# Optimization experiments

Measured on AMD Instinct MI355X. Metric: run time of the kernel, lower is better.

## Reference

```python
import jax, jax.numpy as jnp
import numpy as np

N = 50000      # nodes of type 'student'
E = 625000     # edges per relation
H = 128        # hidden_channels
C = 6          # num_classes
F_IN = 3       # hardcoded num_features in the module


def setup_inputs() -> dict:
    key = jax.random.key(0)
    ks = jax.random.split(key, 32)
    s = 0.05
    d = {}
    d["x_student"] = jax.random.normal(ks[0], (N, F_IN), dtype=jnp.float32)
    d["ei_friend"] = jax.random.randint(ks[1], (2, E), 0, N)
    d["ei_study"] = jax.random.randint(ks[2], (2, E), 0, N)
    # embedding Linear(3 -> H)
    d["emb_w"] = jax.random.normal(ks[3], (F_IN, H), dtype=jnp.float32) * s
    d["emb_b"] = jnp.zeros((H,), jnp.float32)
    # per-layer, per-edge-type RGCNConv params: relation-0 weight, root weight, bias
    i = 4
    for l in range(2):
        for e in ("f", "s"):
            d[f"w_rel_{l}_{e}"] = jax.random.normal(ks[i], (H, H), dtype=jnp.float32) * s; i += 1
            d[f"w_root_{l}_{e}"] = jax.random.normal(ks[i], (H, H), dtype=jnp.float32) * s; i += 1
            d[f"b_{l}_{e}"] = jnp.zeros((H,), jnp.float32)
    # output Linear(H -> C)
    d["out_w"] = jax.random.normal(ks[i], (H, C), dtype=jnp.float32) * s
    d["out_b"] = jnp.zeros((C,), jnp.float32)
    return d


def _rgcn_conv(h, ei, w_rel, w_root, b):
    # PyG RGCNConv with edge_type==0 everywhere: mean-aggregate src features at dst,
    # project by relation-0 weight, add root transform and bias.
    src, dst = ei[0], ei[1]
    msg = h[src]                                             # [E, H] gather
    agg = jax.ops.segment_sum(msg, dst, num_segments=N)      # [N, H]
    deg = jax.ops.segment_sum(jnp.ones((ei.shape[1],), h.dtype), dst, num_segments=N)
    agg = agg / jnp.maximum(deg, 1.0)[:, None]               # mean aggr (0 for isolated nodes)
    return agg @ w_rel + h @ w_root + b


def reference(x_student, ei_friend, ei_study, emb_w, emb_b,
              w_rel_0_f, w_root_0_f, b_0_f, w_rel_0_s, w_root_0_s, b_0_s,
              w_rel_1_f, w_root_1_f, b_1_f, w_rel_1_s, w_root_1_s, b_1_s,
              out_w, out_b):
    h = jax.nn.relu(x_student @ emb_w + emb_b)
    # layer 0: sum over the two relations, divide by valid_edge_count=2, relu (dropout eval=no-op)
    acc = _rgcn_conv(h, ei_friend, w_rel_0_f, w_root_0_f, b_0_f) \
        + _rgcn_conv(h, ei_study, w_rel_0_s, w_root_0_s, b_0_s)
    h = jax.nn.relu(acc / 2.0)
    # layer 1 (last): no relu/dropout
    acc = _rgcn_conv(h, ei_friend, w_rel_1_f, w_root_1_f, b_1_f) \
        + _rgcn_conv(h, ei_study, w_rel_1_s, w_root_1_s, b_1_s)
    h = acc / 2.0
    return h @ out_w + out_b
```

## Files before the change

kernel.cpp:

```cpp
#include <hip/hip_runtime.h>

#define NN 50000
#define NE 625000
#define HD 128
#define CAP 40
#define ZROW NN

typedef __attribute__((ext_vector_type(8))) short short8;
typedef __attribute__((ext_vector_type(4))) float f32x4;
typedef __attribute__((ext_vector_type(4))) unsigned uint4v;

__device__ __forceinline__ unsigned short f2bf(float f) {
    unsigned u = __builtin_bit_cast(unsigned, f);
    u += 0x7FFFu + ((u >> 16) & 1u);
    return (unsigned short)(u >> 16);
}
__device__ __forceinline__ unsigned pack2(float lo, float hi) {
    return (unsigned)f2bf(lo) | ((unsigned)f2bf(hi) << 16);
}
__device__ __forceinline__ float bflo(unsigned v) { unsigned u = v << 16; return __builtin_bit_cast(float, u); }
__device__ __forceinline__ float bfhi(unsigned v) { unsigned u = v & 0xFFFF0000u; return __builtin_bit_cast(float, u); }

__device__ __forceinline__ void extract8(uint4v u, int j0, int cnt, unsigned* out) {
    unsigned raw[8];
    raw[0] = u.x & 0xFFFFu; raw[1] = u.x >> 16;
    raw[2] = u.y & 0xFFFFu; raw[3] = u.y >> 16;
    raw[4] = u.z & 0xFFFFu; raw[5] = u.z >> 16;
    raw[6] = u.w & 0xFFFFu; raw[7] = u.w >> 16;
    #pragma unroll
    for (int j = 0; j < 8; ++j) out[j] = (j0 + j < cnt) ? raw[j] : ZROW;
}

__global__ __launch_bounds__(256) void k_prep(
    const float* __restrict__ x, const float* __restrict__ w,
    const float* __restrict__ b, unsigned* __restrict__ h0, unsigned* __restrict__ h1,
    const int* __restrict__ ei_f, const int* __restrict__ ei_s,
    int* __restrict__ degF, int* __restrict__ degS,
    unsigned short* __restrict__ bktF, unsigned short* __restrict__ bktS,
    const float* __restrict__ wrf0, const float* __restrict__ wtf0, const float* __restrict__ bf0,
    const float* __restrict__ wrs0, const float* __restrict__ wts0, const float* __restrict__ bs0,
    const float* __restrict__ wrf1, const float* __restrict__ wtf1, const float* __restrict__ bf1,
    const float* __restrict__ wrs1, const float* __restrict__ wts1, const float* __restrict__ bs1,
    unsigned short* __restrict__ Wt, float* __restrict__ bcat)
{
    int bid = blockIdx.x, t = threadIdx.x;
    if (bid < 3920) {
        int rel = bid >= 1960;
        int bqq = bid - rel * 1960;
        int cls = bqq & 7;
        int chunk = bqq >> 3;
        const int* ei; int* deg; unsigned short* bkt;
        if (rel == 0) { ei = ei_f; deg = degF; bkt = bktF; }
        else          { ei = ei_s; deg = degS; bkt = bktS; }
        const int lo = cls * 6250, hi = lo + 6250;
        int e0 = chunk * 2560 + t;
        #pragma unroll
        for (int i = 0; i < 10; ++i) {
            int e = e0 + i * 256;
            if (e >= NE) continue;
            int d = ei[NE + e];
            if (d >= lo && d < hi) {
                int s = ei[e];
                int pos = atomicAdd(&deg[d], 1);
                if (pos < CAP) bkt[d*CAP + pos] = (unsigned short)s;
            }
        }
    } else if (bid < 16420) {
        int i = (bid - 3920) * 256 + t;
        int n = i >> 6, c = (i & 63) * 2;
        float x0 = x[n*3+0], x1 = x[n*3+1], x2 = x[n*3+2];
        float v0 = fmaf(x0, w[c],   fmaf(x1, w[HD+c],   fmaf(x2, w[2*HD+c],   b[c])));
        float v1 = fmaf(x0, w[c+1], fmaf(x1, w[HD+c+1], fmaf(x2, w[2*HD+c+1], b[c+1])));
        v0 = fmaxf(v0, 0.f); v1 = fmaxf(v1, 0.f);
        h0[i] = pack2(v0, v1);
    } else if (bid == 16420) {
        if (t < 64)       h0[(long)ZROW*64 + t] = 0u;
        else if (t < 128) h1[(long)ZROW*64 + (t - 64)] = 0u;
    } else {
        int i = (bid - 16421) * 256 + t;
        int ln = i / 384, k = i - ln * 384;
        int l = ln >> 7, n = ln & 127;
        const float* wrf = l ? wrf1 : wrf0;
        const float* wrs = l ? wrs1 : wrs0;
        const float* wtf = l ? wtf1 : wtf0;
        const float* wts = l ? wts1 : wts0;
        float v;
        if (k < 128)      v = wrf[k*HD + n];
        else if (k < 256) v = wrs[(k-128)*HD + n];
        else              v = wtf[(k-256)*HD + n] + wts[(k-256)*HD + n];
        Wt[(long)ln*384 + k] = f2bf(0.5f * v);
        if (i < 256) {
            int ll = i >> 7, cc = i & 127;
            const float* bfp = ll ? bf1 : bf0;
            const float* bsp = ll ? bs1 : bs0;
            bcat[i] = 0.5f * (bfp[cc] + bsp[cc]);
        }
    }
}

__global__ __launch_bounds__(256) void k_spmm(
    const unsigned* __restrict__ h,
    const int* __restrict__ degF, const int* __restrict__ degS,
    const unsigned short* __restrict__ bktF, const unsigned short* __restrict__ bktS,
    unsigned* __restrict__ aggF, unsigned* __restrict__ aggS)
{
    int w = threadIdx.x >> 6, lane = threadIdx.x & 63;
    int n = blockIdx.x * 4 + w;
    int dF = degF[n], dS = degS[n];
    int cF = min(dF, CAP), cS = min(dS, CAP);
    const unsigned short* rowF = bktF + (long)n*CAP;
    const unsigned short* rowS = bktS + (long)n*CAP;
    uint4v uF0 = *(const uint4v*)(rowF);
    uint4v uF1 = *(const uint4v*)(rowF + 8);
    uint4v uS0 = *(const uint4v*)(rowS);
    uint4v uS1 = *(const uint4v*)(rowS + 8);
    unsigned iF[16], iS[16];
    extract8(uF0, 0, cF, iF); extract8(uF1, 8, cF, iF + 8);
    extract8(uS0, 0, cS, iS); extract8(uS1, 8, cS, iS + 8);
    unsigned vF[16], vS[16];
    #pragma unroll
    for (int j = 0; j < 16; ++j) vF[j] = h[iF[j]*64u + lane];
    #pragma unroll
    for (int j = 0; j < 16; ++j) vS[j] = h[iS[j]*64u + lane];
    float aF0 = 0.f, aF1 = 0.f, aS0 = 0.f, aS1 = 0.f;
    #pragma unroll
    for (int j = 0; j < 16; ++j) { aF0 += bflo(vF[j]); aF1 += bfhi(vF[j]); }
    #pragma unroll
    for (int j = 0; j < 16; ++j) { aS0 += bflo(vS[j]); aS1 += bfhi(vS[j]); }
    for (int j = 16; j < cF; j += 8) {
        uint4v u = *(const uint4v*)(rowF + j);
        unsigned ii[8];
        extract8(u, j, cF, ii);
        unsigned vv[8];
        #pragma unroll
        for (int q = 0; q < 8; ++q) vv[q] = h[ii[q]*64u + lane];
        #pragma unroll
        for (int q = 0; q < 8; ++q) { aF0 += bflo(vv[q]); aF1 += bfhi(vv[q]); }
    }
    for (int j = 16; j < cS; j += 8) {
        uint4v u = *(const uint4v*)(rowS + j);
        unsigned ii[8];
        extract8(u, j, cS, ii);
        unsigned vv[8];
        #pragma unroll
        for (int q = 0; q < 8; ++q) vv[q] = h[ii[q]*64u + lane];
        #pragma unroll
        for (int q = 0; q < 8; ++q) { aS0 += bflo(vv[q]); aS1 += bfhi(vv[q]); }
    }
    float invF = 1.f / fmaxf((float)dF, 1.f);
    float invS = 1.f / fmaxf((float)dS, 1.f);
    aggF[n*64 + lane] = pack2(aF0*invF, aF1*invF);
    aggS[n*64 + lane] = pack2(aS0*invS, aS1*invS);
}

__global__ __launch_bounds__(256) void k_gemm(
    const unsigned short* __restrict__ A0, const unsigned short* __restrict__ A1,
    const unsigned short* __restrict__ A2,
    const unsigned short* __restrict__ Wt, const float* __restrict__ bias,
    unsigned short* __restrict__ outH, int mode,
    const float* __restrict__ ow, const float* __restrict__ ob,
    float* __restrict__ out6)
{
    __shared__ unsigned short Bs[16 * 64 * 8];
    const int t = threadIdx.x;
    const int wv = t >> 6, lane = t & 63;
    const int m16 = lane & 15, quad = lane >> 4;
    const int row0 = blockIdx.x * 128 + wv * 32;
    f32x4 acc[2][8];
    #pragma unroll
    for (int mt = 0; mt < 2; ++mt)
        #pragma unroll
        for (int nt = 0; nt < 8; ++nt) acc[mt][nt] = (f32x4){0.f,0.f,0.f,0.f};

    for (int ch = 0; ch < 6; ++ch) {
        const int k0 = ch * 64;
        const unsigned short* src; int kofs;
        if (ch < 2)      { src = A0; kofs = k0; }
        else if (ch < 4) { src = A1; kofs = k0 - 128; }
        else             { src = A2; kofs = k0 - 256; }
        __syncthreads();
        #pragma unroll
        for (int i = 0; i < 4; ++i) {
            int flat = i * 256 + t;
            int fb = flat >> 6, ln = flat & 63;
            int nt = fb >> 1, kc2 = fb & 1;
            int mm = ln & 15, qq = ln >> 4;
            short8 v = *(const short8*)(Wt + (long)(nt*16 + mm)*384 + k0 + kc2*32 + qq*8);
            *(short8*)(Bs + flat*8) = v;
        }
        short8 a[2][2];
        #pragma unroll
        for (int mt = 0; mt < 2; ++mt) {
            int r = row0 + mt*16 + m16;
            #pragma unroll
            for (int kc2 = 0; kc2 < 2; ++kc2) {
                if (r < NN) a[mt][kc2] = *(const short8*)(src + (long)r*HD + kofs + kc2*32 + quad*8);
                else        a[mt][kc2] = short8{0,0,0,0,0,0,0,0};
            }
        }
        __syncthreads();
        #pragma unroll
        for (int kc2 = 0; kc2 < 2; ++kc2)
            #pragma unroll
            for (int nt = 0; nt < 8; ++nt) {
                short8 bfr = *(const short8*)(Bs + ((nt*2 + kc2)*64 + lane)*8);
                acc[0][nt] = __builtin_amdgcn_mfma_f32_16x16x32_bf16(a[0][kc2], bfr, acc[0][nt], 0, 0, 0);
                acc[1][nt] = __builtin_amdgcn_mfma_f32_16x16x32_bf16(a[1][kc2], bfr, acc[1][nt], 0, 0, 0);
            }
    }

    float bs[8];
    #pragma unroll
    for (int nt = 0; nt < 8; ++nt) bs[nt] = bias[nt*16 + m16];

    if (mode == 0) {
        #pragma unroll
        for (int mt = 0; mt < 2; ++mt)
            #pragma unroll
            for (int reg = 0; reg < 4; ++reg) {
                int r = row0 + mt*16 + quad*4 + reg;
                if (r >= NN) continue;
                #pragma unroll
                for (int nt = 0; nt < 8; ++nt) {
                    float v = fmaxf(acc[mt][nt][reg] + bs[nt], 0.f);
                    outH[(long)r*HD + nt*16 + m16] = f2bf(v);
                }
            }
    } else {
        float owr[8][6];
        #pragma unroll
        for (int nt = 0; nt < 8; ++nt) {
            int c = nt*16 + m16;
            #pragma unroll
            for (int j = 0; j < 6; ++j) owr[nt][j] = ow[c*6 + j];
        }
        #pragma unroll
        for (int mt = 0; mt < 2; ++mt)
            #pragma unroll
            for (int reg = 0; reg < 4; ++reg) {
                int r = row0 + mt*16 + quad*4 + reg;
                float tj[6] = {0,0,0,0,0,0};
                #pragma unroll
                for (int nt = 0; nt < 8; ++nt) {
                    float hv = acc[mt][nt][reg] + bs[nt];
                    #pragma unroll
                    for (int j = 0; j < 6; ++j) tj[j] = fmaf(hv, owr[nt][j], tj[j]);
                }
                #pragma unroll
                for (int mask = 1; mask < 16; mask <<= 1)
                    #pragma unroll
                    for (int j = 0; j < 6; ++j) tj[j] += __shfl_xor(tj[j], mask, 64);
                if (m16 == 0 && r < NN) {
                    #pragma unroll
                    for (int j = 0; j < 6; ++j) out6[(long)r*6 + j] = tj[j] + ob[j];
                }
            }
    }
}

extern "C" void kernel_launch(void* const* d_in, const int* in_sizes, int n_in,
                              void* d_out, int out_size, void* d_ws, size_t ws_size,
                              hipStream_t stream)
{
    const float* x     = (const float*)d_in[0];
    const int*   ei_f  = (const int*)d_in[1];
    const int*   ei_s  = (const int*)d_in[2];
    const float* emb_w = (const float*)d_in[3];
    const float* emb_b = (const float*)d_in[4];
    const float* wr0f  = (const float*)d_in[5];
    const float* wt0f  = (const float*)d_in[6];
    const float* b0f   = (const float*)d_in[7];
    const float* wr0s  = (const float*)d_in[8];
    const float* wt0s  = (const float*)d_in[9];
    const float* b0s   = (const float*)d_in[10];
    const float* wr1f  = (const float*)d_in[11];
    const float* wt1f  = (const float*)d_in[12];
    const float* b1f   = (const float*)d_in[13];
    const float* wr1s  = (const float*)d_in[14];
    const float* wt1s  = (const float*)d_in[15];
    const float* b1s   = (const float*)d_in[16];
    const float* out_w = (const float*)d_in[17];
    const float* out_b = (const float*)d_in[18];
    float* out = (float*)d_out;

    char* ws = (char*)d_ws;
    size_t off = 0;
    auto alloc = [&](size_t bytes) { char* p = ws + off; off += (bytes + 255) & ~255ULL; return p; };
    unsigned* h0   = (unsigned*)alloc((size_t)(NN+1)*64*4);
    unsigned* h1   = (unsigned*)alloc((size_t)(NN+1)*64*4);
    unsigned* aggF = (unsigned*)alloc((size_t)NN*64*4);
    unsigned* aggS = (unsigned*)alloc((size_t)NN*64*4);
    int*   degF = (int*)alloc((size_t)NN*4);
    int*   degS = (int*)alloc((size_t)NN*4);
    unsigned short* bktF = (unsigned short*)alloc((size_t)NN*CAP*2);
    unsigned short* bktS = (unsigned short*)alloc((size_t)NN*CAP*2);
    unsigned short* Wt = (unsigned short*)alloc((size_t)2*128*384*2);
    float* bcat = (float*)alloc((size_t)2*HD*4);

    hipMemsetAsync(degF, 0, NN*4, stream);
    hipMemsetAsync(degS, 0, NN*4, stream);

    k_prep<<<16805, 256, 0, stream>>>(x, emb_w, emb_b, h0, h1,
                                      ei_f, ei_s, degF, degS, bktF, bktS,
                                      wr0f, wt0f, b0f, wr0s, wt0s, b0s,
                                      wr1f, wt1f, b1f, wr1s, wt1s, b1s,
                                      Wt, bcat);
    k_spmm<<<NN/4, 256, 0, stream>>>(h0, degF, degS, bktF, bktS, aggF, aggS);
    k_gemm<<<(NN + 127)/128, 256, 0, stream>>>((const unsigned short*)aggF, (const unsigned short*)aggS,
                                               (const unsigned short*)h0, Wt, bcat,
                                               (unsigned short*)h1, 0, out_w, out_b, out);
    k_spmm<<<NN/4, 256, 0, stream>>>(h1, degF, degS, bktF, bktS, aggF, aggS);
    k_gemm<<<(NN + 127)/128, 256, 0, stream>>>((const unsigned short*)aggF, (const unsigned short*)aggS,
                                               (const unsigned short*)h1, Wt + 128*384, bcat + HD,
                                               (unsigned short*)h1, 1, out_w, out_b, out);
}
```

Measured before the change: 276.8 us.

## Fuse embedding into layer-0 aggregation by recomputing from 3-feature inputs

Removes the separate embedding pass from the prep kernel. The first aggregation kernel now gathers each neighbour's 3 raw input features (12 bytes) and recomputes the Linear+ReLU embedding on the fly, in place of gathering 256-byte bf16 hidden rows. It also writes h0 for the root term. This cuts gather bandwidth for layer 0 in exchange for redundant FMA work per edge, and it changes rounding slightly because aggregation now happens in fp32 before the bf16 conversion.

```diff
diff --git a/kernel.cpp b/kernel.cpp
--- a/kernel.cpp
+++ b/kernel.cpp
@@ -32,8 +32,7 @@
 }
 
 __global__ __launch_bounds__(256) void k_prep(
-    const float* __restrict__ x, const float* __restrict__ w,
-    const float* __restrict__ b, unsigned* __restrict__ h0, unsigned* __restrict__ h1,
+    unsigned* __restrict__ h0, unsigned* __restrict__ h1,
     const int* __restrict__ ei_f, const int* __restrict__ ei_s,
     int* __restrict__ degF, int* __restrict__ degS,
     unsigned short* __restrict__ bktF, unsigned short* __restrict__ bktS,
@@ -65,19 +64,11 @@
                 if (pos < CAP) bkt[d*CAP + pos] = (unsigned short)s;
             }
         }
-    } else if (bid < 16420) {
-        int i = (bid - 3920) * 256 + t;
-        int n = i >> 6, c = (i & 63) * 2;
-        float x0 = x[n*3+0], x1 = x[n*3+1], x2 = x[n*3+2];
-        float v0 = fmaf(x0, w[c],   fmaf(x1, w[HD+c],   fmaf(x2, w[2*HD+c],   b[c])));
-        float v1 = fmaf(x0, w[c+1], fmaf(x1, w[HD+c+1], fmaf(x2, w[2*HD+c+1], b[c+1])));
-        v0 = fmaxf(v0, 0.f); v1 = fmaxf(v1, 0.f);
-        h0[i] = pack2(v0, v1);
-    } else if (bid == 16420) {
+    } else if (bid == 3920) {
         if (t < 64)       h0[(long)ZROW*64 + t] = 0u;
         else if (t < 128) h1[(long)ZROW*64 + (t - 64)] = 0u;
     } else {
-        int i = (bid - 16421) * 256 + t;
+        int i = (bid - 3921) * 256 + t;
         int ln = i / 384, k = i - ln * 384;
         int l = ln >> 7, n = ln & 127;
         const float* wrf = l ? wrf1 : wrf0;
@@ -95,6 +86,79 @@
             const float* bsp = ll ? bs1 : bs0;
             bcat[i] = 0.5f * (bfp[cc] + bsp[cc]);
         }
+    }
+}
+
+__global__ __launch_bounds__(256) void k_spmm0(
+    const float* __restrict__ x, const float* __restrict__ ew, const float* __restrict__ eb,
+    const int* __restrict__ degF, const int* __restrict__ degS,
+    const unsigned short* __restrict__ bktF, const unsigned short* __restrict__ bktS,
+    unsigned* __restrict__ aggF, unsigned* __restrict__ aggS, unsigned* __restrict__ h0)
+{
+    int w = threadIdx.x >> 6, lane = threadIdx.x & 63;
+    int n = blockIdx.x * 4 + w;
+    int c = lane * 2;
+    float w00 = ew[c], w01 = ew[c+1];
+    float w10 = ew[HD+c], w11 = ew[HD+c+1];
+    float w20 = ew[2*HD+c], w21 = ew[2*HD+c+1];
+    float b0 = eb[c], b1 = eb[c+1];
+
+    {
+        float x0 = x[n*3], x1 = x[n*3+1], x2 = x[n*3+2];
+        float v0 = fmaxf(fmaf(x0, w00, fmaf(x1, w10, fmaf(x2, w20, b0))), 0.f);
+        float v1 = fmaxf(fmaf(x0, w01, fmaf(x1, w11, fmaf(x2, w21, b1))), 0.f);
+        h0[n*64 + lane] = pack2(v0, v1);
+    }
+
+    #pragma unroll
+    for (int rel = 0; rel < 2; ++rel) {
+        const int* deg = rel ? degS : degF;
+        const unsigned short* bkt = rel ? bktS : bktF;
+        unsigned* agg = rel ? aggS : aggF;
+        int d = deg[n];
+        int cnt = min(d, CAP);
+        const unsigned short* row = bkt + (long)n * CAP;
+        uint4v u0 = *(const uint4v*)(row);
+        uint4v u1 = *(const uint4v*)(row + 8);
+        unsigned raw[16];
+        raw[0] = u0.x & 0xFFFFu; raw[1] = u0.x >> 16;
+        raw[2] = u0.y & 0xFFFFu; raw[3] = u0.y >> 16;
+        raw[4] = u0.z & 0xFFFFu; raw[5] = u0.z >> 16;
+        raw[6] = u0.w & 0xFFFFu; raw[7] = u0.w >> 16;
+        raw[8]  = u1.x & 0xFFFFu; raw[9]  = u1.x >> 16;
+        raw[10] = u1.y & 0xFFFFu; raw[11] = u1.y >> 16;
+        raw[12] = u1.z & 0xFFFFu; raw[13] = u1.z >> 16;
+        raw[14] = u1.w & 0xFFFFu; raw[15] = u1.w >> 16;
+        unsigned idx[16]; float msk[16];
+        #pragma unroll
+        for (int j = 0; j < 16; ++j) {
+            idx[j] = (j < cnt) ? raw[j] : 0u;
+            msk[j] = (j < cnt) ? 1.f : 0.f;
+        }
+        float xr[16][3];
+        #pragma unroll
+        for (int j = 0; j < 16; ++j) {
+            const float* xp = x + idx[j] * 3u;
+            xr[j][0] = xp[0]; xr[j][1] = xp[1]; xr[j][2] = xp[2];
+        }
+        float a0 = 0.f, a1 = 0.f;
+        #pragma unroll
+        for (int j = 0; j < 16; ++j) {
+            float v0 = fmaf(xr[j][0], w00, fmaf(xr[j][1], w10, fmaf(xr[j][2], w20, b0)));
+            float v1 = fmaf(xr[j][0], w01, fmaf(xr[j][1], w11, fmaf(xr[j][2], w21, b1)));
+            a0 += fmaxf(v0, 0.f) * msk[j];
+            a1 += fmaxf(v1, 0.f) * msk[j];
+        }
+        for (int j = 16; j < cnt; ++j) {
+            const float* xp = x + (unsigned)row[j] * 3u;
+            float y0 = xp[0], y1 = xp[1], y2 = xp[2];
+            float v0 = fmaf(y0, w00, fmaf(y1, w10, fmaf(y2, w20, b0)));
+            float v1 = fmaf(y0, w01, fmaf(y1, w11, fmaf(y2, w21, b1)));
+            a0 += fmaxf(v0, 0.f);
+            a1 += fmaxf(v1, 0.f);
+        }
+        float inv = 1.f / fmaxf((float)d, 1.f);
+        agg[n*64 + lane] = pack2(a0 * inv, a1 * inv);
     }
 }
 
@@ -300,12 +364,13 @@
     hipMemsetAsync(degF, 0, NN*4, stream);
     hipMemsetAsync(degS, 0, NN*4, stream);
 
-    k_prep<<<16805, 256, 0, stream>>>(x, emb_w, emb_b, h0, h1,
-                                      ei_f, ei_s, degF, degS, bktF, bktS,
-                                      wr0f, wt0f, b0f, wr0s, wt0s, b0s,
-                                      wr1f, wt1f, b1f, wr1s, wt1s, b1s,
-                                      Wt, bcat);
-    k_spmm<<<NN/4, 256, 0, stream>>>(h0, degF, degS, bktF, bktS, aggF, aggS);
+    k_prep<<<4305, 256, 0, stream>>>(h0, h1,
+                                     ei_f, ei_s, degF, degS, bktF, bktS,
+                                     wr0f, wt0f, b0f, wr0s, wt0s, b0s,
+                                     wr1f, wt1f, b1f, wr1s, wt1s, b1s,
+                                     Wt, bcat);
+    k_spmm0<<<NN/4, 256, 0, stream>>>(x, emb_w, emb_b, degF, degS, bktF, bktS,
+                                      aggF, aggS, h0);
     k_gemm<<<(NN + 127)/128, 256, 0, stream>>>((const unsigned short*)aggF, (const unsigned short*)aggS,
                                                (const unsigned short*)h0, Wt, bcat,
                                                (unsigned short*)h1, 0, out_w, out_b, out);
```

Result: slower. 300.1 us (+8.4%).

## Read GEMM weights directly from global memory and shrink per-wave row tile

Applied to the files above, without the earlier changes.

The fused dense GEMM no longer stages weight fragments in shared memory with block barriers. Each MFMA B-fragment is now loaded straight from global memory, relying on L1/L2 caching of the small weight matrix. Each wave now covers 16 rows instead of 32, and the grid doubles to 64 rows per block. This removes LDS traffic and __syncthreads stalls and raises the number of blocks. In exchange, weight fragments are fetched redundantly by every wave, with no reuse across two row tiles, which increases cache and memory-request pressure.

```diff
diff --git a/kernel.cpp b/kernel.cpp
--- a/kernel.cpp
+++ b/kernel.cpp
@@ -161,71 +161,47 @@
     const float* __restrict__ ow, const float* __restrict__ ob,
     float* __restrict__ out6)
 {
-    __shared__ unsigned short Bs[16 * 64 * 8];
-    const int t = threadIdx.x;
-    const int wv = t >> 6, lane = t & 63;
+    const int wv = threadIdx.x >> 6, lane = threadIdx.x & 63;
     const int m16 = lane & 15, quad = lane >> 4;
-    const int row0 = blockIdx.x * 128 + wv * 32;
-    f32x4 acc[2][8];
-    #pragma unroll
-    for (int mt = 0; mt < 2; ++mt)
-        #pragma unroll
-        for (int nt = 0; nt < 8; ++nt) acc[mt][nt] = (f32x4){0.f,0.f,0.f,0.f};
-
-    for (int ch = 0; ch < 6; ++ch) {
-        const int k0 = ch * 64;
+    const int row0 = blockIdx.x * 64 + wv * 16;
+    f32x4 acc[8];
+    #pragma unroll
+    for (int nt = 0; nt < 8; ++nt) acc[nt] = (f32x4){0.f,0.f,0.f,0.f};
+
+    const int r = row0 + m16;
+    const bool valid = r < NN;
+
+    #pragma unroll
+    for (int kc = 0; kc < 12; ++kc) {
         const unsigned short* src; int kofs;
-        if (ch < 2)      { src = A0; kofs = k0; }
-        else if (ch < 4) { src = A1; kofs = k0 - 128; }
-        else             { src = A2; kofs = k0 - 256; }
-        __syncthreads();
-        #pragma unroll
-        for (int i = 0; i < 4; ++i) {
-            int flat = i * 256 + t;
-            int fb = flat >> 6, ln = flat & 63;
-            int nt = fb >> 1, kc2 = fb & 1;
-            int mm = ln & 15, qq = ln >> 4;
-            short8 v = *(const short8*)(Wt + (long)(nt*16 + mm)*384 + k0 + kc2*32 + qq*8);
-            *(short8*)(Bs + flat*8) = v;
-        }
-        short8 a[2][2];
-        #pragma unroll
-        for (int mt = 0; mt < 2; ++mt) {
-            int r = row0 + mt*16 + m16;
-            #pragma unroll
-            for (int kc2 = 0; kc2 < 2; ++kc2) {
-                if (r < NN) a[mt][kc2] = *(const short8*)(src + (long)r*HD + kofs + kc2*32 + quad*8);
-                else        a[mt][kc2] = short8{0,0,0,0,0,0,0,0};
-            }
-        }
-        __syncthreads();
-        #pragma unroll
-        for (int kc2 = 0; kc2 < 2; ++kc2)
+        if (kc < 4)      { src = A0; kofs = kc*32; }
+        else if (kc < 8) { src = A1; kofs = kc*32 - 128; }
+        else             { src = A2; kofs = kc*32 - 256; }
+        short8 a;
+        if (valid) a = *(const short8*)(src + (long)r*HD + kofs + quad*8);
+        else       a = short8{0,0,0,0,0,0,0,0};
+        #pragma unroll
+        for (int nt = 0; nt < 8; ++nt) {
+            short8 bfr = *(const short8*)(Wt + (long)(nt*16 + m16)*384 + kc*32 + quad*8);
+            acc[nt] = __builtin_amdgcn_mfma_f32_16x16x32_bf16(a, bfr, acc[nt], 0, 0, 0);
+        }
+    }
+
+    float bs[8];
+    #pragma unroll
+    for (int nt = 0; nt < 8; ++nt) bs[nt] = bias[nt*16 + m16];
+
+    if (mode == 0) {
+        #pragma unroll
+        for (int reg = 0; reg < 4; ++reg) {
+            int rr = row0 + quad*4 + reg;
+            if (rr >= NN) continue;
             #pragma unroll
             for (int nt = 0; nt < 8; ++nt) {
-                short8 bfr = *(const short8*)(Bs + ((nt*2 + kc2)*64 + lane)*8);
-                acc[0][nt] = __builtin_amdgcn_mfma_f32_16x16x32_bf16(a[0][kc2], bfr, acc[0][nt], 0, 0, 0);
-                acc[1][nt] = __builtin_amdgcn_mfma_f32_16x16x32_bf16(a[1][kc2], bfr, acc[1][nt], 0, 0, 0);
-            }
-    }
-
-    float bs[8];
-    #pragma unroll
-    for (int nt = 0; nt < 8; ++nt) bs[nt] = bias[nt*16 + m16];
-
-    if (mode == 0) {
-        #pragma unroll
-        for (int mt = 0; mt < 2; ++mt)
-            #pragma unroll
-            for (int reg = 0; reg < 4; ++reg) {
-                int r = row0 + mt*16 + quad*4 + reg;
-                if (r >= NN) continue;
-                #pragma unroll
-                for (int nt = 0; nt < 8; ++nt) {
-                    float v = fmaxf(acc[mt][nt][reg] + bs[nt], 0.f);
-                    outH[(long)r*HD + nt*16 + m16] = f2bf(v);
-                }
-            }
+                float v = fmaxf(acc[nt][reg] + bs[nt], 0.f);
+                outH[(long)rr*HD + nt*16 + m16] = f2bf(v);
+            }
+        }
     } else {
         float owr[8][6];
         #pragma unroll
@@ -235,26 +211,24 @@
             for (int j = 0; j < 6; ++j) owr[nt][j] = ow[c*6 + j];
         }
         #pragma unroll
-        for (int mt = 0; mt < 2; ++mt)
-            #pragma unroll
-            for (int reg = 0; reg < 4; ++reg) {
-                int r = row0 + mt*16 + quad*4 + reg;
-                float tj[6] = {0,0,0,0,0,0};
+        for (int reg = 0; reg < 4; ++reg) {
+            int rr = row0 + quad*4 + reg;
+            float tj[6] = {0,0,0,0,0,0};
+            #pragma unroll
+            for (int nt = 0; nt < 8; ++nt) {
+                float hv = acc[nt][reg] + bs[nt];
                 #pragma unroll
-                for (int nt = 0; nt < 8; ++nt) {
-                    float hv = acc[mt][nt][reg] + bs[nt];
-                    #pragma unroll
-                    for (int j = 0; j < 6; ++j) tj[j] = fmaf(hv, owr[nt][j], tj[j]);
-                }
+                for (int j = 0; j < 6; ++j) tj[j] = fmaf(hv, owr[nt][j], tj[j]);
+            }
+            #pragma unroll
+            for (int mask = 1; mask < 16; mask <<= 1)
                 #pragma unroll
-                for (int mask = 1; mask < 16; mask <<= 1)
-                    #pragma unroll
-                    for (int j = 0; j < 6; ++j) tj[j] += __shfl_xor(tj[j], mask, 64);
-                if (m16 == 0 && r < NN) {
-                    #pragma unroll
-                    for (int j = 0; j < 6; ++j) out6[(long)r*6 + j] = tj[j] + ob[j];
-                }
-            }
+                for (int j = 0; j < 6; ++j) tj[j] += __shfl_xor(tj[j], mask, 64);
+            if (m16 == 0 && rr < NN) {
+                #pragma unroll
+                for (int j = 0; j < 6; ++j) out6[(long)rr*6 + j] = tj[j] + ob[j];
+            }
+        }
     }
 }
 
@@ -306,11 +280,11 @@
                                       wr1f, wt1f, b1f, wr1s, wt1s, b1s,
                                       Wt, bcat);
     k_spmm<<<NN/4, 256, 0, stream>>>(h0, degF, degS, bktF, bktS, aggF, aggS);
-    k_gemm<<<(NN + 127)/128, 256, 0, stream>>>((const unsigned short*)aggF, (const unsigned short*)aggS,
-                                               (const unsigned short*)h0, Wt, bcat,
-                                               (unsigned short*)h1, 0, out_w, out_b, out);
+    k_gemm<<<(NN + 63)/64, 256, 0, stream>>>((const unsigned short*)aggF, (const unsigned short*)aggS,
+                                             (const unsigned short*)h0, Wt, bcat,
+                                             (unsigned short*)h1, 0, out_w, out_b, out);
     k_spmm<<<NN/4, 256, 0, stream>>>(h1, degF, degS, bktF, bktS, aggF, aggS);
-    k_gemm<<<(NN + 127)/128, 256, 0, stream>>>((const unsigned short*)aggF, (const unsigned short*)aggS,
-                                               (const unsigned short*)h1, Wt + 128*384, bcat + HD,
-                                               (unsigned short*)h1, 1, out_w, out_b, out);
-}
+    k_gemm<<<(NN + 63)/64, 256, 0, stream>>>((const unsigned short*)aggF, (const unsigned short*)aggS,
+                                             (const unsigned short*)h1, Wt + 128*384, bcat + HD,
+                                             (unsigned short*)h1, 1, out_w, out_b, out);
+}
```

Measured after the change: 340.5 us. 1.23x slower.
